# Kernel tuning notes

Hardware: AMD Instinct MI355X
Metric: run time of the kernel (lower is better)

The kernel has to match this reference:

```python
import jax, jax.numpy as jnp
import numpy as np

NUM_HEADS = 8
MAXN = 1.0 - 1e-5        # ball projection radius for |k|=1
ATANH_CLIP = 1.0 - 1e-7  # artanh argument clamp (geoopt-style)
MIN_DEN = 1e-15

def _sqnorm(x):
    return jnp.sum(x * x, axis=-1, keepdims=True)

def _norm(x):
    return jnp.sqrt(jnp.clip(_sqnorm(x), MIN_DEN))

def artanh(x):
    return jnp.arctanh(jnp.clip(x, -ATANH_CLIP, ATANH_CLIP))

def project(x):
    n = _norm(x)
    return jnp.where(n > MAXN, x * (MAXN / n), x)

def mobius_add(x, y):
    # Mobius addition on Poincare ball, k=-1
    x2, y2 = _sqnorm(x), _sqnorm(y)
    xy = jnp.sum(x * y, axis=-1, keepdims=True)
    num = (1.0 + 2.0 * xy + y2) * x + (1.0 - x2) * y
    den = 1.0 + 2.0 * xy + x2 * y2
    return num / jnp.maximum(den, MIN_DEN)

def mobius_matvec(W, x):
    xn = jnp.clip(_norm(x), MIN_DEN)
    mx = x @ W.T
    mxn = jnp.clip(_norm(mx), MIN_DEN)
    res = jnp.tanh(mxn / xn * artanh(xn)) * (mx / mxn)
    zero = jnp.all(mx == 0, axis=-1, keepdims=True)
    return jnp.where(zero, jnp.zeros_like(res), res)

def mobius_linear(x, W, b):
    return project(mobius_add(mobius_matvec(W, x), b))

def logmap0(y):
    yn = jnp.clip(_norm(y), MIN_DEN)
    return artanh(yn) * y / yn

def expmap0(u):
    un = jnp.clip(_norm(u), MIN_DEN)
    return jnp.tanh(un) * u / un

def _fwd(query, key, value, Wq, bq, Wk, bk, Wv, bv, Wo, bo):
    B, S, D = query.shape
    dk = D // NUM_HEADS
    heads = lambda x: x.reshape(B, S, NUM_HEADS, dk).transpose(0, 2, 1, 3)
    Q = heads(mobius_linear(query, Wq, bq))  # (B,H,S,dk)
    K = heads(mobius_linear(key, Wk, bk))
    V = heads(mobius_linear(value, Wv, bv))
    # pairwise Poincare distance dist(q,k) = 2*artanh(||(-q) (+) k||),
    # expanded via dot products so we never build a (B,H,S,S,dk) tensor
    x2 = _sqnorm(Q)                          # (B,H,S,1)
    y2 = jnp.swapaxes(_sqnorm(K), -1, -2)    # (B,H,1,S)
    xy = jnp.einsum('bhid,bhjd->bhij', Q, K)
    A = 1.0 - 2.0 * xy + y2                  # coeff of (-q)
    Bc = 1.0 - x2                            # coeff of k
    num2 = A * A * x2 + Bc * Bc * y2 - 2.0 * A * Bc * xy
    den = jnp.maximum(1.0 - 2.0 * xy + x2 * y2, MIN_DEN)
    dist = 2.0 * artanh(jnp.sqrt(jnp.clip(num2, 0.0)) / den)
    scores = -dist / np.sqrt(dk).astype(np.float32)
    attn = jax.nn.softmax(scores, axis=-1)   # dropout skipped (eval/deterministic)
    # gyromidpoint weighted sum (vectorized form of the original python loops):
    # all softmax weights are > 0, so every j passes the >1e-10 branch
    w = attn / (jnp.sum(attn, axis=-1, keepdims=True) + 1e-10)
    mid = jnp.einsum('bhij,bhjd->bhid', w, logmap0(V))
    out = expmap0(mid)
    out = out.transpose(0, 2, 1, 3).reshape(B, S, D)
    return mobius_linear(out, Wo, bo), attn


def setup_inputs() -> dict:
    key = jax.random.key(0)
    ks = jax.random.split(key, 12)
    B, S, D = 2, 2048, 512
    pt = lambda k: project(0.05 * jax.random.normal(k, (B, S, D), dtype=jnp.float32))
    inp = {'query': pt(ks[0]), 'key': pt(ks[1]), 'value': pt(ks[2])}
    wscale = 1.0 / np.sqrt(D)
    for i, nm in enumerate(['q', 'k', 'v', 'o']):
        inp['W' + nm] = wscale * jax.random.normal(ks[3 + i], (D, D), dtype=jnp.float32)
        inp['b' + nm] = project(0.01 * jax.random.normal(ks[7 + i], (D,), dtype=jnp.float32))
    return inp


def reference(query, key, value, Wq, bq, Wk, bk, Wv, bv, Wo, bo):
    return _fwd(query, key, value, Wq, bq, Wk, bk, Wv, bv, Wo, bo)
```

## Files before the change

kernel.cpp:

```cpp
#include <hip/hip_runtime.h>
#include <math.h>

namespace {

constexpr int kB  = 2;
constexpr int kS  = 2048;
constexpr int kD  = 512;
constexpr int kH  = 8;
constexpr int kDK = 64;
constexpr int kM  = kB * kS;
constexpr int kBH = kB * kH;

typedef __attribute__((ext_vector_type(8))) short bf16x8;
typedef __attribute__((ext_vector_type(4))) float f32x4;

__device__ __forceinline__ float wave_sum64(float v) {
#pragma unroll
    for (int o = 32; o > 0; o >>= 1) v += __shfl_xor(v, o, 64);
    return v;
}

__device__ __forceinline__ unsigned short f2bf(float f) {
    unsigned u = __float_as_uint(f);
    unsigned r = (u + 0x7FFF + ((u >> 16) & 1)) >> 16;
    return (unsigned short)r;
}
__device__ __forceinline__ float bf2f(unsigned short h) {
    return __uint_as_float(((unsigned)h) << 16);
}

__device__ __forceinline__ bf16x8 mk_bf8(unsigned p0, unsigned p1) {
    union { unsigned u[4]; bf16x8 v; } t;
    t.u[0] = p0; t.u[1] = p1; t.u[2] = 0; t.u[3] = 0;
    return t.v;
}

#define MAXN_F  ((float)(1.0 - 1e-5))
#define ACLIP_F ((float)(1.0 - 1e-7))

__global__ __launch_bounds__(256) void gemm_mfma(const float* __restrict__ X,
                                                 const float* __restrict__ W,
                                                 float* __restrict__ Y) {
    __shared__ unsigned short Ah[64 * 64], Al[64 * 64], Bh[64 * 64], Bl[64 * 64];
    const int m0 = blockIdx.x * 64;
    const int n0 = blockIdx.y * 64;
    const int tid = threadIdx.x;
    const int w = tid >> 6, l = tid & 63;
    const int lr = l & 15, lh = l >> 4;
    const int sr = tid >> 2;
    const int sk = (tid & 3) * 16;
    float4 xr[4], wr[4];
#pragma unroll
    for (int i = 0; i < 4; ++i) {
        xr[i] = *(const float4*)(X + (size_t)(m0 + sr) * 512 + sk + i * 4);
        wr[i] = *(const float4*)(W + (size_t)(n0 + sr) * 512 + sk + i * 4);
    }
    f32x4 acc[4];
#pragma unroll
    for (int j = 0; j < 4; ++j) acc[j] = (f32x4){0.f, 0.f, 0.f, 0.f};

    for (int c = 0; c < 8; ++c) {
        if (c) __syncthreads();
        {
            unsigned hx[8], lx[8], hw_[8], lw_[8];
#pragma unroll
            for (int t = 0; t < 8; ++t) {
                float e0 = ((const float*)&xr[t >> 1])[(t & 1) * 2 + 0];
                float e1 = ((const float*)&xr[t >> 1])[(t & 1) * 2 + 1];
                unsigned short h0 = f2bf(e0), h1 = f2bf(e1);
                hx[t] = (unsigned)h0 | ((unsigned)h1 << 16);
                lx[t] = (unsigned)f2bf(e0 - bf2f(h0)) | ((unsigned)f2bf(e1 - bf2f(h1)) << 16);
                float f0 = ((const float*)&wr[t >> 1])[(t & 1) * 2 + 0];
                float f1 = ((const float*)&wr[t >> 1])[(t & 1) * 2 + 1];
                unsigned short g0 = f2bf(f0), g1 = f2bf(f1);
                hw_[t] = (unsigned)g0 | ((unsigned)g1 << 16);
                lw_[t] = (unsigned)f2bf(f0 - bf2f(g0)) | ((unsigned)f2bf(f1 - bf2f(g1)) << 16);
            }
            const int ga = (sk >> 3) ^ (sr & 7);
            const int gb = ((sk >> 3) + 1) ^ (sr & 7);
            *(uint4*)&Ah[sr * 64 + ga * 8] = make_uint4(hx[0], hx[1], hx[2], hx[3]);
            *(uint4*)&Ah[sr * 64 + gb * 8] = make_uint4(hx[4], hx[5], hx[6], hx[7]);
            *(uint4*)&Al[sr * 64 + ga * 8] = make_uint4(lx[0], lx[1], lx[2], lx[3]);
            *(uint4*)&Al[sr * 64 + gb * 8] = make_uint4(lx[4], lx[5], lx[6], lx[7]);
            *(uint4*)&Bh[sr * 64 + ga * 8] = make_uint4(hw_[0], hw_[1], hw_[2], hw_[3]);
            *(uint4*)&Bh[sr * 64 + gb * 8] = make_uint4(hw_[4], hw_[5], hw_[6], hw_[7]);
            *(uint4*)&Bl[sr * 64 + ga * 8] = make_uint4(lw_[0], lw_[1], lw_[2], lw_[3]);
            *(uint4*)&Bl[sr * 64 + gb * 8] = make_uint4(lw_[4], lw_[5], lw_[6], lw_[7]);
        }
        if (c < 7) {
            const int k1 = (c + 1) * 64;
#pragma unroll
            for (int i = 0; i < 4; ++i) {
                xr[i] = *(const float4*)(X + (size_t)(m0 + sr) * 512 + k1 + sk + i * 4);
                wr[i] = *(const float4*)(W + (size_t)(n0 + sr) * 512 + k1 + sk + i * 4);
            }
        }
        __syncthreads();
#pragma unroll
        for (int ks = 0; ks < 2; ++ks) {
            const int kb = ks * 4 + lh;
            const int row = w * 16 + lr;
            const int aoff = row * 64 + ((kb ^ (row & 7)) << 3);
            bf16x8 ah = *(const bf16x8*)&Ah[aoff];
            bf16x8 al = *(const bf16x8*)&Al[aoff];
#pragma unroll
            for (int fn = 0; fn < 4; ++fn) {
                const int col = fn * 16 + lr;
                const int boff = col * 64 + ((kb ^ (col & 7)) << 3);
                bf16x8 bh8 = *(const bf16x8*)&Bh[boff];
                bf16x8 bl8 = *(const bf16x8*)&Bl[boff];
                acc[fn] = __builtin_amdgcn_mfma_f32_16x16x32_bf16(ah, bh8, acc[fn], 0, 0, 0);
                acc[fn] = __builtin_amdgcn_mfma_f32_16x16x32_bf16(al, bh8, acc[fn], 0, 0, 0);
                acc[fn] = __builtin_amdgcn_mfma_f32_16x16x32_bf16(ah, bl8, acc[fn], 0, 0, 0);
            }
        }
    }
#pragma unroll
    for (int fn = 0; fn < 4; ++fn)
#pragma unroll
        for (int r = 0; r < 4; ++r)
            Y[(size_t)(m0 + w * 16 + lh * 4 + r) * 512 + n0 + fn * 16 + lr] = acc[fn][r];
}

__global__ __launch_bounds__(256) void rowops(const float* __restrict__ X,
                                              const float* __restrict__ MX,
                                              const float* __restrict__ bvec,
                                              float* __restrict__ out) {
    __shared__ float4 red4[4];
    __shared__ float red1[4];
    const int row = blockIdx.x;
    const int tid = threadIdx.x;
    const float2 xv = ((const float2*)(X + (size_t)row * kD))[tid];
    const float2 mv = ((const float2*)(MX + (size_t)row * kD))[tid];
    const float2 bv = ((const float2*)bvec)[tid];
    float sx  = fmaf(xv.x, xv.x, xv.y * xv.y);
    float sm  = fmaf(mv.x, mv.x, mv.y * mv.y);
    float smb = fmaf(mv.x, bv.x, mv.y * bv.y);
    float sb  = fmaf(bv.x, bv.x, bv.y * bv.y);
#pragma unroll
    for (int o = 32; o > 0; o >>= 1) {
        sx  += __shfl_xor(sx, o, 64);
        sm  += __shfl_xor(sm, o, 64);
        smb += __shfl_xor(smb, o, 64);
        sb  += __shfl_xor(sb, o, 64);
    }
    if ((tid & 63) == 0) red4[tid >> 6] = make_float4(sx, sm, smb, sb);
    __syncthreads();
    {
        float4 r0 = red4[0], r1 = red4[1], r2 = red4[2], r3 = red4[3];
        sx  = r0.x + r1.x + r2.x + r3.x;
        sm  = r0.y + r1.y + r2.y + r3.y;
        smb = r0.z + r1.z + r2.z + r3.z;
        sb  = r0.w + r1.w + r2.w + r3.w;
    }
    float xn  = sqrtf(fmaxf(sx, 1e-15f));
    float mxn = sqrtf(fmaxf(sm, 1e-15f));
    float xc  = fminf(xn, ACLIP_F);
    float at  = 0.5f * logf((1.f + xc) / (1.f - xc));
    float sc  = tanhf(mxn / xn * at) / mxn;
    if (sm == 0.f) sc = 0.f;
    float x2 = sc * sc * sm;
    float xy = sc * smb;
    float y2 = sb;
    float c1 = 1.f + 2.f * xy + y2;
    float c2 = 1.f - x2;
    float den = fmaxf(1.f + 2.f * xy + x2 * y2, 1e-15f);
    float idn = 1.f / den;
    float ux = (c1 * sc * mv.x + c2 * bv.x) * idn;
    float uy = (c1 * sc * mv.y + c2 * bv.y) * idn;
    float su = wave_sum64(fmaf(ux, ux, uy * uy));
    if ((tid & 63) == 0) red1[tid >> 6] = su;
    __syncthreads();
    su = (red1[0] + red1[1]) + (red1[2] + red1[3]);
    float n = sqrtf(fmaxf(su, 1e-15f));
    float f = (n > MAXN_F) ? (MAXN_F / n) : 1.f;
    ((float2*)(out + (size_t)row * kD))[tid] = make_float2(ux * f, uy * f);
}

__global__ __launch_bounds__(256) void prep2(const float* __restrict__ Qp,
                                             const float* __restrict__ Kp,
                                             const float* __restrict__ Vp,
                                             float* __restrict__ qn2,
                                             float* __restrict__ kn2,
                                             unsigned short* __restrict__ LVbT) {
    __shared__ unsigned short T[64][66];
    const int bh = blockIdx.x >> 5;
    const int k0 = (blockIdx.x & 31) * 64;
    const int b = bh >> 3, h = bh & 7;
    const int w = threadIdx.x >> 6, l = threadIdx.x & 63;
#pragma unroll 4
    for (int i = 0; i < 16; ++i) {
        const int s = k0 + w * 16 + i;
        const size_t src = (size_t)(b * kS + s) * kD + h * kDK + l;
        float qv = Qp[src], kv = Kp[src], vv = Vp[src];
        float sq = wave_sum64(qv * qv);
        float sk = wave_sum64(kv * kv);
        float sv = wave_sum64(vv * vv);
        if (l == 0) { qn2[(bh << 11) + s] = sq; kn2[(bh << 11) + s] = sk; }
        float yn = sqrtf(fmaxf(sv, 1e-15f));
        float yc = fminf(yn, ACLIP_F);
        float coef = 0.5f * logf((1.f + yc) / (1.f - yc)) / yn;
        T[l][w * 16 + i] = f2bf(vv * coef);
    }
    __syncthreads();
    const int n = threadIdx.x >> 2, kk = (threadIdx.x & 3) * 16;
    const unsigned int* Tr = (const unsigned int*)&T[n][kk];
    unsigned int u0 = Tr[0], u1 = Tr[1], u2 = Tr[2], u3 = Tr[3];
    unsigned int u4 = Tr[4], u5 = Tr[5], u6 = Tr[6], u7 = Tr[7];
    unsigned short* dst = LVbT + (((size_t)(bh * 64 + n)) << 11) + k0 + kk;
    *(uint4*)dst = make_uint4(u0, u1, u2, u3);
    *(uint4*)(dst + 8) = make_uint4(u4, u5, u6, u7);
}

__global__ __launch_bounds__(256) void split_qk(const float* __restrict__ Qp,
                                                const float* __restrict__ Kp,
                                                unsigned short* __restrict__ Qhi,
                                                unsigned short* __restrict__ Qlo,
                                                unsigned short* __restrict__ Khi,
                                                unsigned short* __restrict__ Klo) {
    const int gid  = blockIdx.x * 4 + (threadIdx.x >> 6);
    const int lane = threadIdx.x & 63;
    const int bh = gid >> 11, s = gid & 2047;
    const int b = bh >> 3, h = bh & 7;
    const size_t src = (size_t)(b * kS + s) * kD + h * kDK + lane;
    const size_t dst = ((size_t)gid << 6) + lane;
    float qv = Qp[src];
    unsigned short qh = f2bf(qv);
    Qhi[dst] = qh;
    Qlo[dst] = f2bf(qv - bf2f(qh));
    float kv = Kp[src];
    unsigned short kh = f2bf(kv);
    Khi[dst] = kh;
    Klo[dst] = f2bf(kv - bf2f(kh));
}

__global__ __launch_bounds__(256) void fused_attn(const unsigned short* __restrict__ Qhi,
                                                  const unsigned short* __restrict__ Qlo,
                                                  const unsigned short* __restrict__ Khi,
                                                  const unsigned short* __restrict__ Klo,
                                                  const unsigned short* __restrict__ LVbT,
                                                  const float* __restrict__ qn2,
                                                  const float* __restrict__ kn2,
                                                  float* __restrict__ attn,
                                                  float* __restrict__ outcat) {
    __shared__ unsigned long long smem_raw[4096];
    unsigned short* KshH = (unsigned short*)smem_raw;
    unsigned short* KshL = KshH + 4096;
    unsigned short* LVsh = KshL + 4096;
    unsigned short* Psh  = LVsh + 4096;
    float* Pmid = (float*)smem_raw;
    __shared__ float rsL[4][32];
    __shared__ float invSL[32];
    unsigned short* eattn = (unsigned short*)attn;

    const int wgid = blockIdx.x;
    const int x = wgid & 7, bq_ = wgid >> 3;
    const int bh = 2 * x + (bq_ >> 6);
    const int i0 = (bq_ & 63) * 32;
    const int b = bh >> 3, h = bh & 7;
    const int tid = threadIdx.x;
    const int w = tid >> 6, l = tid & 63;
    const int lr = l & 15, lh = l >> 4;
    const int srj = tid >> 2;
    const int skk = (tid & 3) * 16;
    const size_t kvbase = ((size_t)(bh << 11)) << 6;
    const size_t lvbase = ((size_t)bh) << 17;

    bf16x8 qah[2][2], qal[2][2];
#pragma unroll
    for (int fm = 0; fm < 2; ++fm)
#pragma unroll
        for (int ks = 0; ks < 2; ++ks) {
            const size_t a = ((size_t)(bh << 11) + i0 + fm * 16 + lr) * 64 + (ks * 4 + lh) * 8;
            qah[fm][ks] = *(const bf16x8*)&Qhi[a];
            qal[fm][ks] = *(const bf16x8*)&Qlo[a];
        }
    float x2s[2];
    x2s[0] = qn2[(bh << 11) + i0 + 0 * 16 + lr];
    x2s[1] = qn2[(bh << 11) + i0 + 1 * 16 + lr];

    const int ga = (((skk >> 3) ^ (srj & 7)) << 3);
    const int gb = ((((skk >> 3) + 1) ^ (srj & 7)) << 3);
    const int jrow = w * 16 + lr;
    const int aoff0 = jrow * 64;
    uint4 pA0, pA1, pB0, pB1, pC0, pC1;
    {
        const unsigned short* kh = Khi + kvbase + (size_t)srj * 64 + skk;
        const unsigned short* kl = Klo + kvbase + (size_t)srj * 64 + skk;
        const unsigned short* lv = LVbT + lvbase + (size_t)srj * 2048 + skk;
        pA0 = *(const uint4*)kh; pA1 = *(const uint4*)(kh + 8);
        pB0 = *(const uint4*)kl; pB1 = *(const uint4*)(kl + 8);
        pC0 = *(const uint4*)lv; pC1 = *(const uint4*)(lv + 8);
    }

    f32x4 pvacc[2][4];
#pragma unroll
    for (int fm = 0; fm < 2; ++fm)
#pragma unroll
        for (int g2 = 0; g2 < 4; ++g2) pvacc[fm][g2] = (f32x4){0.f, 0.f, 0.f, 0.f};
    float rsp[2] = {0.f, 0.f};

    const int fl_row = tid >> 3, fl_g = tid & 7;
    const int pgj = w * 2 + (lh >> 1);
    const int pjo = (lh & 1) * 4;

    for (int t = 0; t < 32; ++t) {
        const int j0 = t * 64;
        __syncthreads();
        if (t) {
            uint4 ev = *(const uint4*)&Psh[fl_row * 64 + ((fl_g ^ (fl_row & 7)) << 3)];
            *(uint4*)(eattn + ((size_t)(bh << 11) + i0 + fl_row) * 4096 +
                      (j0 - 64) + fl_g * 8) = ev;
        }
        *(uint4*)&KshH[srj * 64 + ga] = pA0; *(uint4*)&KshH[srj * 64 + gb] = pA1;
        *(uint4*)&KshL[srj * 64 + ga] = pB0; *(uint4*)&KshL[srj * 64 + gb] = pB1;
        *(uint4*)&LVsh[srj * 64 + ga] = pC0; *(uint4*)&LVsh[srj * 64 + gb] = pC1;
        if (t < 31) {
            const unsigned short* kh = Khi + kvbase + (size_t)(j0 + 64 + srj) * 64 + skk;
            const unsigned short* kl = Klo + kvbase + (size_t)(j0 + 64 + srj) * 64 + skk;
            const unsigned short* lv = LVbT + lvbase + (size_t)srj * 2048 + j0 + 64 + skk;
            pA0 = *(const uint4*)kh; pA1 = *(const uint4*)(kh + 8);
            pB0 = *(const uint4*)kl; pB1 = *(const uint4*)(kl + 8);
            pC0 = *(const uint4*)lv; pC1 = *(const uint4*)(lv + 8);
        }
        __syncthreads();
        f32x4 sacc[2];
        sacc[0] = (f32x4){0.f, 0.f, 0.f, 0.f};
        sacc[1] = (f32x4){0.f, 0.f, 0.f, 0.f};
#pragma unroll
        for (int ks = 0; ks < 2; ++ks) {
            const int kb = ks * 4 + lh;
            const int aoff = aoff0 + ((kb ^ (jrow & 7)) << 3);
            bf16x8 kh8 = *(const bf16x8*)&KshH[aoff];
            bf16x8 kl8 = *(const bf16x8*)&KshL[aoff];
#pragma unroll
            for (int fm = 0; fm < 2; ++fm) {
                sacc[fm] = __builtin_amdgcn_mfma_f32_16x16x32_bf16(kh8, qah[fm][ks], sacc[fm], 0, 0, 0);
                sacc[fm] = __builtin_amdgcn_mfma_f32_16x16x32_bf16(kh8, qal[fm][ks], sacc[fm], 0, 0, 0);
                sacc[fm] = __builtin_amdgcn_mfma_f32_16x16x32_bf16(kl8, qah[fm][ks], sacc[fm], 0, 0, 0);
            }
        }
        float4 y2v = *(const float4*)(kn2 + (bh << 11) + j0 + w * 16 + lh * 4);
        bf16x8 ebf[2];
#pragma unroll
        for (int fm = 0; fm < 2; ++fm) {
            const float x2 = x2s[fm];
            float es[4];
#pragma unroll
            for (int r = 0; r < 4; ++r) {
                float xy = sacc[fm][r];
                float y2 = ((const float*)&y2v)[r];
                float A_ = 1.f - 2.f * xy + y2;
                float Bc = 1.f - x2;
                float num2 = A_ * A_ * x2 + Bc * Bc * y2 - 2.f * A_ * Bc * xy;
                float den  = fmaxf(1.f - 2.f * xy + x2 * y2, 1e-15f);
                float sn   = __builtin_amdgcn_sqrtf(fmaxf(num2, 0.f));
                float dm   = den - sn;
                dm = fmaxf(dm, (den + sn) * 5e-8f);
                float rr = (den + sn) * __builtin_amdgcn_rcpf(dm);
                float e = __builtin_amdgcn_exp2f(-0.125f * __builtin_amdgcn_logf(rr));
                es[r] = e;
                rsp[fm] += e;
            }
            unsigned p0 = (unsigned)f2bf(es[0]) | ((unsigned)f2bf(es[1]) << 16);
            unsigned p1 = (unsigned)f2bf(es[2]) | ((unsigned)f2bf(es[3]) << 16);
            ebf[fm] = mk_bf8(p0, p1);
            const int prow = fm * 16 + lr;
            *(uint2*)&Psh[prow * 64 + ((pgj ^ (prow & 7)) << 3) + pjo] = make_uint2(p0, p1);
        }
#pragma unroll
        for (int g2 = 0; g2 < 4; ++g2) {
            const int dk = g2 * 16 + lr;
            uint2 lvp = *(const uint2*)&LVsh[dk * 64 + ((pgj ^ (dk & 7)) << 3) + pjo];
            bf16x8 bfr = mk_bf8(lvp.x, lvp.y);
            pvacc[0][g2] = __builtin_amdgcn_mfma_f32_16x16x32_bf16(ebf[0], bfr, pvacc[0][g2], 0, 0, 0);
            pvacc[1][g2] = __builtin_amdgcn_mfma_f32_16x16x32_bf16(ebf[1], bfr, pvacc[1][g2], 0, 0, 0);
        }
    }
    __syncthreads();
    {
        uint4 ev = *(const uint4*)&Psh[fl_row * 64 + ((fl_g ^ (fl_row & 7)) << 3)];
        *(uint4*)(eattn + ((size_t)(bh << 11) + i0 + fl_row) * 4096 + 31 * 64 + fl_g * 8) = ev;
    }
#pragma unroll
    for (int fm = 0; fm < 2; ++fm) {
        rsp[fm] += __shfl_xor(rsp[fm], 16, 64);
        rsp[fm] += __shfl_xor(rsp[fm], 32, 64);
    }
    __syncthreads();
    if (l < 16) { rsL[w][l] = rsp[0]; rsL[w][16 + l] = rsp[1]; }
#pragma unroll
    for (int fm = 0; fm < 2; ++fm)
#pragma unroll
        for (int g2 = 0; g2 < 4; ++g2)
#pragma unroll
            for (int r = 0; r < 4; ++r)
                Pmid[w * 2048 + (fm * 16 + lh * 4 + r) * 64 + g2 * 16 + lr] = pvacc[fm][g2][r];
    __syncthreads();
    if (tid < 32)
        invSL[tid] = 1.f / (rsL[0][tid] + rsL[1][tid] + rsL[2][tid] + rsL[3][tid]);
    __syncthreads();
    {
        const int q = tid >> 3;
        const int c8 = (tid & 7) * 8;
        float m[8];
#pragma unroll
        for (int i = 0; i < 8; i += 4) {
            float4 a0 = *(const float4*)&Pmid[0 * 2048 + q * 64 + c8 + i];
            float4 a1 = *(const float4*)&Pmid[1 * 2048 + q * 64 + c8 + i];
            float4 a2 = *(const float4*)&Pmid[2 * 2048 + q * 64 + c8 + i];
            float4 a3 = *(const float4*)&Pmid[3 * 2048 + q * 64 + c8 + i];
            m[i + 0] = (a0.x + a1.x) + (a2.x + a3.x);
            m[i + 1] = (a0.y + a1.y) + (a2.y + a3.y);
            m[i + 2] = (a0.z + a1.z) + (a2.z + a3.z);
            m[i + 3] = (a0.w + a1.w) + (a2.w + a3.w);
        }
        const float is = invSL[q];
        float ns = 0.f;
#pragma unroll
        for (int i = 0; i < 8; ++i) { m[i] *= is; ns = fmaf(m[i], m[i], ns); }
        ns += __shfl_xor(ns, 1, 64);
        ns += __shfl_xor(ns, 2, 64);
        ns += __shfl_xor(ns, 4, 64);
        float un = sqrtf(fmaxf(ns, 1e-15f));
        float coef = tanhf(un) / un;
        float* dst = outcat + (size_t)(b * kS + i0 + q) * kD + h * kDK + c8;
        *(float4*)dst       = make_float4(m[0] * coef, m[1] * coef, m[2] * coef, m[3] * coef);
        *(float4*)(dst + 4) = make_float4(m[4] * coef, m[5] * coef, m[6] * coef, m[7] * coef);
    }
    for (int r = 0; r < 32; r += 2) {
        const size_t rb0 = (size_t)(bh << 11) + i0 + r;
        const size_t rb1 = rb0 + 1;
        uint4 ev0 = *(const uint4*)(eattn + rb0 * 4096 + tid * 8);
        uint4 ev1 = *(const uint4*)(eattn + rb1 * 4096 + tid * 8);
        const float is0 = invSL[r];
        const float is1 = invSL[r + 1];
        __syncthreads();
        float o[8];
        o[0] = __uint_as_float(ev0.x << 16) * is0;
        o[1] = __uint_as_float(ev0.x & 0xFFFF0000u) * is0;
        o[2] = __uint_as_float(ev0.y << 16) * is0;
        o[3] = __uint_as_float(ev0.y & 0xFFFF0000u) * is0;
        o[4] = __uint_as_float(ev0.z << 16) * is0;
        o[5] = __uint_as_float(ev0.z & 0xFFFF0000u) * is0;
        o[6] = __uint_as_float(ev0.w << 16) * is0;
        o[7] = __uint_as_float(ev0.w & 0xFFFF0000u) * is0;
        float* d0 = attn + rb0 * kS + tid * 8;
        *(float4*)d0       = make_float4(o[0], o[1], o[2], o[3]);
        *(float4*)(d0 + 4) = make_float4(o[4], o[5], o[6], o[7]);
        o[0] = __uint_as_float(ev1.x << 16) * is1;
        o[1] = __uint_as_float(ev1.x & 0xFFFF0000u) * is1;
        o[2] = __uint_as_float(ev1.y << 16) * is1;
        o[3] = __uint_as_float(ev1.y & 0xFFFF0000u) * is1;
        o[4] = __uint_as_float(ev1.z << 16) * is1;
        o[5] = __uint_as_float(ev1.z & 0xFFFF0000u) * is1;
        o[6] = __uint_as_float(ev1.w << 16) * is1;
        o[7] = __uint_as_float(ev1.w & 0xFFFF0000u) * is1;
        float* d1 = attn + rb1 * kS + tid * 8;
        *(float4*)d1       = make_float4(o[0], o[1], o[2], o[3]);
        *(float4*)(d1 + 4) = make_float4(o[4], o[5], o[6], o[7]);
    }
}

}

extern "C" void kernel_launch(void* const* d_in, const int* in_sizes, int n_in,
                              void* d_out, int out_size, void* d_ws, size_t ws_size,
                              hipStream_t stream) {
    const float* q  = (const float*)d_in[0];
    const float* k  = (const float*)d_in[1];
    const float* v  = (const float*)d_in[2];
    const float* Wq = (const float*)d_in[3];
    const float* bq = (const float*)d_in[4];
    const float* Wk = (const float*)d_in[5];
    const float* bk = (const float*)d_in[6];
    const float* Wv = (const float*)d_in[7];
    const float* bv = (const float*)d_in[8];
    const float* Wo = (const float*)d_in[9];
    const float* bo = (const float*)d_in[10];

    float* out  = (float*)d_out;
    float* attn = out + (size_t)kM * kD;

    constexpr size_t NBUF = (size_t)kM * kD;
    float* ws  = (float*)d_ws;
    float* A0  = ws;
    float* A1  = ws + NBUF;
    float* A2  = ws + 2 * NBUF;
    float* A3  = ws + 3 * NBUF;
    float* qn2 = ws + 4 * NBUF;
    float* kn2 = qn2 + (size_t)kBH * kS;

    constexpr size_t HP = (size_t)kBH * kS * kDK;
    unsigned short* Qhi = (unsigned short*)A2;
    unsigned short* Qlo = Qhi + HP;
    unsigned short* Khi = (unsigned short*)out;
    unsigned short* Klo = Khi + HP;
    unsigned short* LVbT = (unsigned short*)A3;

    dim3 gg(kM / 64, kD / 64);

    gemm_mfma<<<gg, 256, 0, stream>>>(q, Wq, A3);
    rowops<<<kM, 256, 0, stream>>>(q, A3, bq, A0);
    gemm_mfma<<<gg, 256, 0, stream>>>(k, Wk, A3);
    rowops<<<kM, 256, 0, stream>>>(k, A3, bk, A1);
    gemm_mfma<<<gg, 256, 0, stream>>>(v, Wv, A3);
    rowops<<<kM, 256, 0, stream>>>(v, A3, bv, A2);

    prep2<<<kBH * 32, 256, 0, stream>>>(A0, A1, A2, qn2, kn2, LVbT);

    split_qk<<<(kBH * kS) / 4, 256, 0, stream>>>(A0, A1, Qhi, Qlo, Khi, Klo);

    fused_attn<<<kBH * (kS / 32), 256, 0, stream>>>(Qhi, Qlo, Khi, Klo, LVbT,
                                                    qn2, kn2, attn, A1);

    gemm_mfma<<<gg, 256, 0, stream>>>(A1, Wo, A2);
    rowops<<<kM, 256, 0, stream>>>(A1, A2, bo, out);
}
```

Before: 278.8 us.

## Batch Q/K/V projections into single launches and fold split_qk into prep

Runs the three input projection GEMMs and their row-wise Mobius ops as single launches, with the projection selected by a grid z/y dimension. Scratch buffers are remapped into the attn output region so all three results can live at once. The bf16 hi/lo split of Q and K moves into the prep kernel, so the separate split_qk pass and its extra read of Q and K go away. The goal is fewer launches and larger grids that fill the GPU better. The cost is more live scratch memory and the split's stores now coming from the prep kernel's per-row loop.

```diff
diff --git a/kernel.cpp b/kernel.cpp
--- a/kernel.cpp
+++ b/kernel.cpp
@@ -38,13 +38,11 @@
 #define MAXN_F  ((float)(1.0 - 1e-5))
 #define ACLIP_F ((float)(1.0 - 1e-7))
 
-__global__ __launch_bounds__(256) void gemm_mfma(const float* __restrict__ X,
-                                                 const float* __restrict__ W,
-                                                 float* __restrict__ Y) {
+__device__ __forceinline__ void gemm_body(const float* __restrict__ X,
+                                          const float* __restrict__ W,
+                                          float* __restrict__ Y,
+                                          int m0, int n0, int tid) {
     __shared__ unsigned short Ah[64 * 64], Al[64 * 64], Bh[64 * 64], Bl[64 * 64];
-    const int m0 = blockIdx.x * 64;
-    const int n0 = blockIdx.y * 64;
-    const int tid = threadIdx.x;
     const int w = tid >> 6, l = tid & 63;
     const int lr = l & 15, lh = l >> 4;
     const int sr = tid >> 2;
@@ -122,14 +120,33 @@
             Y[(size_t)(m0 + w * 16 + lh * 4 + r) * 512 + n0 + fn * 16 + lr] = acc[fn][r];
 }
 
-__global__ __launch_bounds__(256) void rowops(const float* __restrict__ X,
-                                              const float* __restrict__ MX,
-                                              const float* __restrict__ bvec,
-                                              float* __restrict__ out) {
+__global__ __launch_bounds__(256) void gemm_mfma(const float* __restrict__ X,
+                                                 const float* __restrict__ W,
+                                                 float* __restrict__ Y) {
+    gemm_body(X, W, Y, blockIdx.x * 64, blockIdx.y * 64, threadIdx.x);
+}
+
+__global__ __launch_bounds__(256) void gemm_mfma3(const float* __restrict__ X0,
+                                                  const float* __restrict__ X1,
+                                                  const float* __restrict__ X2,
+                                                  const float* __restrict__ W0,
+                                                  const float* __restrict__ W1,
+                                                  const float* __restrict__ W2,
+                                                  float* __restrict__ Y0,
+                                                  float* __restrict__ Y1,
+                                                  float* __restrict__ Y2) {
+    const float* X = (blockIdx.z == 0) ? X0 : (blockIdx.z == 1) ? X1 : X2;
+    const float* W = (blockIdx.z == 0) ? W0 : (blockIdx.z == 1) ? W1 : W2;
+    float*       Y = (blockIdx.z == 0) ? Y0 : (blockIdx.z == 1) ? Y1 : Y2;
+    gemm_body(X, W, Y, blockIdx.x * 64, blockIdx.y * 64, threadIdx.x);
+}
+
+__device__ __forceinline__ void rowops_body(const float* __restrict__ X,
+                                            const float* __restrict__ MX,
+                                            const float* __restrict__ bvec,
+                                            float* __restrict__ out, int row, int tid) {
     __shared__ float4 red4[4];
     __shared__ float red1[4];
-    const int row = blockIdx.x;
-    const int tid = threadIdx.x;
     const float2 xv = ((const float2*)(X + (size_t)row * kD))[tid];
     const float2 mv = ((const float2*)(MX + (size_t)row * kD))[tid];
     const float2 bv = ((const float2*)bvec)[tid];
@@ -177,12 +194,43 @@
     ((float2*)(out + (size_t)row * kD))[tid] = make_float2(ux * f, uy * f);
 }
 
-__global__ __launch_bounds__(256) void prep2(const float* __restrict__ Qp,
+__global__ __launch_bounds__(256) void rowops(const float* __restrict__ X,
+                                              const float* __restrict__ MX,
+                                              const float* __restrict__ bvec,
+                                              float* __restrict__ out) {
+    rowops_body(X, MX, bvec, out, blockIdx.x, threadIdx.x);
+}
+
+__global__ __launch_bounds__(256) void rowops3(const float* __restrict__ X0,
+                                               const float* __restrict__ X1,
+                                               const float* __restrict__ X2,
+                                               const float* __restrict__ MX0,
+                                               const float* __restrict__ MX1,
+                                               const float* __restrict__ MX2,
+                                               const float* __restrict__ b0,
+                                               const float* __restrict__ b1,
+                                               const float* __restrict__ b2,
+                                               float* __restrict__ o0,
+                                               float* __restrict__ o1,
+                                               float* __restrict__ o2) {
+    const int z = blockIdx.y;
+    const float* X  = (z == 0) ? X0  : (z == 1) ? X1  : X2;
+    const float* MX = (z == 0) ? MX0 : (z == 1) ? MX1 : MX2;
+    const float* bv = (z == 0) ? b0  : (z == 1) ? b1  : b2;
+    float*       o  = (z == 0) ? o0  : (z == 1) ? o1  : o2;
+    rowops_body(X, MX, bv, o, blockIdx.x, threadIdx.x);
+}
+
+__global__ __launch_bounds__(256) void prep3(const float* __restrict__ Qp,
                                              const float* __restrict__ Kp,
                                              const float* __restrict__ Vp,
                                              float* __restrict__ qn2,
                                              float* __restrict__ kn2,
-                                             unsigned short* __restrict__ LVbT) {
+                                             unsigned short* __restrict__ LVbT,
+                                             unsigned short* __restrict__ Qhi,
+                                             unsigned short* __restrict__ Qlo,
+                                             unsigned short* __restrict__ Khi,
+                                             unsigned short* __restrict__ Klo) {
     __shared__ unsigned short T[64][66];
     const int bh = blockIdx.x >> 5;
     const int k0 = (blockIdx.x & 31) * 64;
@@ -192,7 +240,14 @@
     for (int i = 0; i < 16; ++i) {
         const int s = k0 + w * 16 + i;
         const size_t src = (size_t)(b * kS + s) * kD + h * kDK + l;
+        const size_t gdst = (((size_t)(bh << 11) + s) << 6) + l;
         float qv = Qp[src], kv = Kp[src], vv = Vp[src];
+        unsigned short qh = f2bf(qv);
+        Qhi[gdst] = qh;
+        Qlo[gdst] = f2bf(qv - bf2f(qh));
+        unsigned short kh = f2bf(kv);
+        Khi[gdst] = kh;
+        Klo[gdst] = f2bf(kv - bf2f(kh));
         float sq = wave_sum64(qv * qv);
         float sk = wave_sum64(kv * kv);
         float sv = wave_sum64(vv * vv);
@@ -210,28 +265,6 @@
     unsigned short* dst = LVbT + (((size_t)(bh * 64 + n)) << 11) + k0 + kk;
     *(uint4*)dst = make_uint4(u0, u1, u2, u3);
     *(uint4*)(dst + 8) = make_uint4(u4, u5, u6, u7);
-}
-
-__global__ __launch_bounds__(256) void split_qk(const float* __restrict__ Qp,
-                                                const float* __restrict__ Kp,
-                                                unsigned short* __restrict__ Qhi,
-                                                unsigned short* __restrict__ Qlo,
-                                                unsigned short* __restrict__ Khi,
-                                                unsigned short* __restrict__ Klo) {
-    const int gid  = blockIdx.x * 4 + (threadIdx.x >> 6);
-    const int lane = threadIdx.x & 63;
-    const int bh = gid >> 11, s = gid & 2047;
-    const int b = bh >> 3, h = bh & 7;
-    const size_t src = (size_t)(b * kS + s) * kD + h * kDK + lane;
-    const size_t dst = ((size_t)gid << 6) + lane;
-    float qv = Qp[src];
-    unsigned short qh = f2bf(qv);
-    Qhi[dst] = qh;
-    Qlo[dst] = f2bf(qv - bf2f(qh));
-    float kv = Kp[src];
-    unsigned short kh = f2bf(kv);
-    Khi[dst] = kh;
-    Klo[dst] = f2bf(kv - bf2f(kh));
 }
 
 __global__ __launch_bounds__(256) void fused_attn(const unsigned short* __restrict__ Qhi,
@@ -491,6 +524,11 @@
     float* qn2 = ws + 4 * NBUF;
     float* kn2 = qn2 + (size_t)kBH * kS;
 
+    float* mxq  = A3;
+    float* mxk  = attn;
+    float* mxv  = attn + NBUF;
+    float* VpBuf = attn + 2 * NBUF;
+
     constexpr size_t HP = (size_t)kBH * kS * kDK;
     unsigned short* Qhi = (unsigned short*)A2;
     unsigned short* Qlo = Qhi + HP;
@@ -499,17 +537,14 @@
     unsigned short* LVbT = (unsigned short*)A3;
 
     dim3 gg(kM / 64, kD / 64);
-
-    gemm_mfma<<<gg, 256, 0, stream>>>(q, Wq, A3);
-    rowops<<<kM, 256, 0, stream>>>(q, A3, bq, A0);
-    gemm_mfma<<<gg, 256, 0, stream>>>(k, Wk, A3);
-    rowops<<<kM, 256, 0, stream>>>(k, A3, bk, A1);
-    gemm_mfma<<<gg, 256, 0, stream>>>(v, Wv, A3);
-    rowops<<<kM, 256, 0, stream>>>(v, A3, bv, A2);
-
-    prep2<<<kBH * 32, 256, 0, stream>>>(A0, A1, A2, qn2, kn2, LVbT);
-
-    split_qk<<<(kBH * kS) / 4, 256, 0, stream>>>(A0, A1, Qhi, Qlo, Khi, Klo);
+    dim3 gg3(kM / 64, kD / 64, 3);
+    dim3 rr3(kM, 3);
+
+    gemm_mfma3<<<gg3, 256, 0, stream>>>(q, k, v, Wq, Wk, Wv, mxq, mxk, mxv);
+    rowops3<<<rr3, 256, 0, stream>>>(q, k, v, mxq, mxk, mxv, bq, bk, bv, A0, A1, VpBuf);
+
+    prep3<<<kBH * 32, 256, 0, stream>>>(A0, A1, VpBuf, qn2, kn2, LVbT,
+                                        Qhi, Qlo, Khi, Klo);
 
     fused_attn<<<kBH * (kS / 32), 256, 0, stream>>>(Qhi, Qlo, Khi, Klo, LVbT,
                                                     qn2, kn2, attn, A1);
```

New measurement: 259.6 us (median of 2 runs). -6.9%, faster.
